# Performance work log

Measured on AMD Instinct MI355X. Metric: run time of the kernel, lower is better.

Reference implementation:

```python
import jax, jax.numpy as jnp
import numpy as np

INPUT_DIM = 1024
OUTPUT_DIM = 1000
DEPTH = 10
LAMBDA_REG = 1e-3
N_INTERNAL = 2 ** DEPTH - 1
N_LEAF = 2 ** DEPTH
BATCH = 16384


def setup_inputs() -> dict:
    key = jax.random.key(0)
    k1, k2, k3 = jax.random.split(key, 3)
    X = jax.random.normal(k1, (BATCH, INPUT_DIM), dtype=jnp.float32)
    # torch nn.Linear weight layout: [out_features, in_features]; scaled to keep
    # sigmoid routing probs away from 0/1 saturation (log-reg term).
    W_internal = jax.random.normal(k2, (N_INTERNAL, INPUT_DIM + 1), dtype=jnp.float32) * 0.02
    W_leaf = jax.random.normal(k3, (OUTPUT_DIM, N_LEAF), dtype=jnp.float32) * 0.02
    return {"X": X, "W_internal": W_internal, "W_leaf": W_leaf}


def _tree_paths(X, W_internal):
    B = X.shape[0]
    Xb = jnp.concatenate([jnp.ones((B, 1), X.dtype), X], axis=1)  # [B, D+1]
    logits = jax.nn.sigmoid(Xb @ W_internal.T)                    # [B, N_int]
    routing = jnp.stack([logits, 1.0 - logits], axis=2)           # [B, N_int, 2]
    path = jnp.ones((B, 1), X.dtype)
    reg = jnp.float32(0.0)
    start = 0
    for layer in range(DEPTH):
        n = 2 ** layer
        lp = routing[:, start:start + n, :].reshape(B, 2 * n)     # next_paths [B, 2n]
        path = jnp.repeat(path, 2, axis=1) * lp                   # new path probs [B, 2n]
        # Faithful to source: parent_idx = node_idx // 2 indexes the UPDATED path probs.
        parent = jnp.repeat(path[:, :n], 2, axis=1)               # [B, 2n]
        num = jnp.sum(lp * parent, axis=0)                        # [2n]
        den = jnp.sum(parent, axis=0) + 1e-8                      # [2n]
        alpha = num / den
        factor = LAMBDA_REG * 2.0 ** (-layer)
        reg = reg + factor * jnp.sum(-0.5 * (jnp.log(alpha) + jnp.log(1.0 - alpha)))
        start += n
    return path, reg  # path: [B, 2^DEPTH]


def reference(X, W_internal, W_leaf):
    path_probs, reg = _tree_paths(X, W_internal)
    predictions = path_probs @ W_leaf.T   # [B, output_dim]
    return predictions, reg
```

## Files before the change

kernel.cpp:

```cpp
#include <hip/hip_runtime.h>
#include <hip/hip_bf16.h>

#define B_ROWS 16384
#define K_DIM  1024
#define N_INT  1023
#define N_OUT  1000

using s8vec = __attribute__((ext_vector_type(8))) short;
using f32x4 = __attribute__((ext_vector_type(4))) float;

static const size_t OFF_XB   = 0;
static const size_t OFF_W1   = OFF_XB   + 33554432;
static const size_t OFF_BIAS = OFF_W1   + 2097152;
static const size_t OFF_PROB = OFF_BIAS + 4096;
static const size_t OFF_PATH = OFF_PROB + 33554432;
static const size_t OFF_W2   = OFF_PATH + 33554432;
static const size_t OFF_SG   = OFF_W2   + 2097152;

__device__ __forceinline__ float b2f(ushort u) {
  return __uint_as_float(((unsigned)u) << 16);
}
__device__ __forceinline__ float blo(unsigned u) { return __uint_as_float(u << 16); }
__device__ __forceinline__ float bhi(unsigned u) { return __uint_as_float(u & 0xffff0000u); }
__device__ __forceinline__ ushort f2b(float f) {
  unsigned u = __float_as_uint(f);
  u = u + 0x7FFFu + ((u >> 16) & 1u);
  return (ushort)(u >> 16);
}

__device__ __forceinline__ void load_lds16(const ushort* g, ushort* l) {
  __builtin_amdgcn_global_load_lds((const __attribute__((address_space(1))) void*)g,
                                   (__attribute__((address_space(3))) void*)l,
                                   16, 0, 0);
}

__global__ __launch_bounds__(256) void cvt_all(const float4* __restrict__ X,
                                               ushort4* __restrict__ O,
                                               const float* __restrict__ Wi,
                                               const float* __restrict__ Wl,
                                               ushort* __restrict__ W1,
                                               ushort* __restrict__ W2,
                                               float* __restrict__ bias) {
  const int b = blockIdx.x;
  if (b < 16384) {
    const int i = b * 256 + threadIdx.x;
    const float4 v = X[i];
    ushort4 o;
    o.x = f2b(v.x); o.y = f2b(v.y); o.z = f2b(v.z); o.w = f2b(v.w);
    O[i] = o;
  } else {
    const int idx = (b - 16384) * 256 + threadIdx.x;
    if (idx < (1 << 20)) {
      const int n = idx >> 10, k = idx & 1023;
      const float v = (n < N_INT) ? Wi[n * 1025 + 1 + k] : 0.f;
      W1[idx] = f2b(v);
      if (k == 0) bias[n] = (n < N_INT) ? Wi[n * 1025] : 0.f;
    } else {
      const int j = idx - (1 << 20);
      const int n = j >> 10, k = j & 1023;
      const float v = (n < N_OUT) ? Wl[n * 1024 + k] : 0.f;
      W2[j] = f2b(v);
    }
  }
}

template <int MODE>
__global__ __launch_bounds__(256, 4) void gemm_bt(const ushort* __restrict__ A,
                                                  const ushort* __restrict__ Bm,
                                                  const float* __restrict__ bias,
                                                  void* __restrict__ outp) {
  __shared__ ushort As[4096];
  __shared__ ushort Bs[4096];
  const int tid = threadIdx.x;
  const int bm = blockIdx.x, bn = blockIdx.y;
  const int lane = tid & 63, wv = tid >> 6;
  const int wm = wv >> 1, wn = wv & 1;
  const int m16 = lane & 15, q = lane >> 4;
  const int qs = q ^ ((m16 >> 1) & 3);

  const int r0 = tid >> 2;
  const int qsw = (tid & 3) ^ ((r0 >> 1) & 3);
  const ushort* aG = A  + (size_t)(bm * 128 + r0) * 1024 + qsw * 8;
  const ushort* bG = Bm + (size_t)(bn * 128 + r0) * 1024 + qsw * 8;
  ushort* AsW = As + wv * 512;
  ushort* BsW = Bs + wv * 512;

  f32x4 acc[4][4] = {};

  for (int k0 = 0; k0 < 1024; k0 += 32) {
    if (k0) __syncthreads();
    load_lds16(aG + k0, AsW);
    load_lds16(aG + 65536 + k0, AsW + 2048);
    load_lds16(bG + k0, BsW);
    load_lds16(bG + 65536 + k0, BsW + 2048);
    __syncthreads();

    s8vec af[4], bfv[4];
#pragma unroll
    for (int i = 0; i < 4; ++i)
      af[i] = *(const s8vec*)(As + (wm * 64 + i * 16 + m16) * 32 + qs * 8);
#pragma unroll
    for (int j = 0; j < 4; ++j)
      bfv[j] = *(const s8vec*)(Bs + (wn * 64 + j * 16 + m16) * 32 + qs * 8);
#pragma unroll
    for (int i = 0; i < 4; ++i)
#pragma unroll
      for (int j = 0; j < 4; ++j)
        acc[i][j] = __builtin_amdgcn_mfma_f32_16x16x32_bf16(af[i], bfv[j], acc[i][j], 0, 0, 0);
  }

  if (MODE == 0) {
    ushort* P = (ushort*)outp;
#pragma unroll
    for (int i = 0; i < 4; ++i)
#pragma unroll
      for (int r = 0; r < 4; ++r) {
        const int gr = bm * 128 + wm * 64 + i * 16 + q * 4 + r;
#pragma unroll
        for (int j = 0; j < 4; ++j) {
          const int gc = bn * 128 + wn * 64 + j * 16 + m16;
          const float z = acc[i][j][r] + bias[gc];
          const float p = 1.f / (1.f + expf(-z));
          if (gc < N_INT) P[(size_t)gr * 1024 + gc + 1] = f2b(p);
        }
      }
  } else {
    float* O = (float*)outp;
#pragma unroll
    for (int i = 0; i < 4; ++i)
#pragma unroll
      for (int r = 0; r < 4; ++r) {
        const int gr = bm * 128 + wm * 64 + i * 16 + q * 4 + r;
#pragma unroll
        for (int j = 0; j < 4; ++j) {
          const int gc = bn * 128 + wn * 64 + j * 16 + m16;
          if (gc < N_OUT) O[(size_t)gr * 1000 + gc] = acc[i][j][r];
        }
      }
  }
}

__global__ __launch_bounds__(256) void tree_kernel(const ushort* __restrict__ probs,
                                                   ushort* __restrict__ path,
                                                   float* __restrict__ Spart) {
  __shared__ float Ss[4096];
  for (int i = threadIdx.x; i < 4096; i += 256) Ss[i] = 0.f;
  __syncthreads();
  const int lane = threadIdx.x & 63;
  const int gw = blockIdx.x * 4 + (threadIdx.x >> 6);

  float at1[6] = {}, at2[6] = {};
  float ae1[30] = {}, ae2[30] = {};

  ushort h4[2], p6a[2]; uint p7a[2]; uint2 p8a[2]; uint4 p9a[2];
#pragma unroll
  for (int rr = 0; rr < 2; ++rr) {
    const ushort* prow = probs + (size_t)(gw * 2 + rr) * 1024;
    h4[rr]  = prow[lane];
    p6a[rr] = prow[64 + lane];
    p7a[rr] = *(const uint*)(prow + 128 + 2 * lane);
    p8a[rr] = *(const uint2*)(prow + 256 + 4 * lane);
    p9a[rr] = *(const uint4*)(prow + 512 + 8 * lane);
  }

#pragma unroll
  for (int rr = 0; rr < 2; ++rr) {
    const int r = gw * 2 + rr;
    const int hh = (int)h4[rr];
    const ushort p6 = p6a[rr];
    const uint   p7 = p7a[rr];
    const uint2  p8 = p8a[rr];
    const uint4  p9 = p9a[rr];

    float v = 1.f;
#pragma unroll
    for (int t = 1; t <= 6; ++t) {
      const int ell = t - 1;
      const int e = lane >> (6 - t);
      const float p = b2f((ushort)__shfl(hh, (1 << ell) + (e >> 1)));
      v *= (e & 1) ? (1.f - p) : p;
      const float pj = b2f((ushort)__shfl(hh, ((1 << ell) + e) & 63));
      if (((lane & ((1 << (6 - t)) - 1)) == 0) && (e < (1 << ell))) {
        at1[ell] += v;
        at2[ell] += pj * v;
      }
    }

    float w[16];
    {
      const float p = b2f(p6);
      w[1] = v * (1.f - p); w[0] = v * p;
    }
    {
      const int j0 = __shfl((int)p6, 2 * lane);
      const int j1 = __shfl((int)p6, 2 * lane + 1);
      if (lane < 32) {
        ae1[0] += w[0]; ae2[0] += b2f((ushort)j0) * w[0];
        ae1[1] += w[1]; ae2[1] += b2f((ushort)j1) * w[1];
      }
    }
    {
      const float pA = blo(p7), pB = bhi(p7);
      w[3] = w[1] * (1.f - pB); w[2] = w[1] * pB;
      w[1] = w[0] * (1.f - pA); w[0] = w[0] * pA;
    }
    {
      const uint ua = (uint)__shfl((int)p7, 2 * lane);
      const uint ub = (uint)__shfl((int)p7, 2 * lane + 1);
      if (lane < 32) {
        ae1[2] += w[0]; ae2[2] += blo(ua) * w[0];
        ae1[3] += w[1]; ae2[3] += bhi(ua) * w[1];
        ae1[4] += w[2]; ae2[4] += blo(ub) * w[2];
        ae1[5] += w[3]; ae2[5] += bhi(ub) * w[3];
      }
    }
    {
      const float pv[4] = { blo(p8.x), bhi(p8.x), blo(p8.y), bhi(p8.y) };
#pragma unroll
      for (int i = 3; i >= 0; --i) {
        w[2 * i + 1] = w[i] * (1.f - pv[i]);
        w[2 * i]     = w[i] * pv[i];
      }
    }
    {
      const uint u0 = (uint)__shfl((int)p8.x, 2 * lane);
      const uint u1 = (uint)__shfl((int)p8.y, 2 * lane);
      const uint u2 = (uint)__shfl((int)p8.x, 2 * lane + 1);
      const uint u3 = (uint)__shfl((int)p8.y, 2 * lane + 1);
      if (lane < 32) {
        ae1[6]  += w[0]; ae2[6]  += blo(u0) * w[0];
        ae1[7]  += w[1]; ae2[7]  += bhi(u0) * w[1];
        ae1[8]  += w[2]; ae2[8]  += blo(u1) * w[2];
        ae1[9]  += w[3]; ae2[9]  += bhi(u1) * w[3];
        ae1[10] += w[4]; ae2[10] += blo(u2) * w[4];
        ae1[11] += w[5]; ae2[11] += bhi(u2) * w[5];
        ae1[12] += w[6]; ae2[12] += blo(u3) * w[6];
        ae1[13] += w[7]; ae2[13] += bhi(u3) * w[7];
      }
    }
    {
      const uint pv[4] = { p9.x, p9.y, p9.z, p9.w };
#pragma unroll
      for (int i = 7; i >= 0; --i) {
        const float p = (i & 1) ? bhi(pv[i >> 1]) : blo(pv[i >> 1]);
        w[2 * i + 1] = w[i] * (1.f - p);
        w[2 * i]     = w[i] * p;
      }
    }
    {
      uint s_[8];
      s_[0] = (uint)__shfl((int)p9.x, 2 * lane);
      s_[1] = (uint)__shfl((int)p9.y, 2 * lane);
      s_[2] = (uint)__shfl((int)p9.z, 2 * lane);
      s_[3] = (uint)__shfl((int)p9.w, 2 * lane);
      s_[4] = (uint)__shfl((int)p9.x, 2 * lane + 1);
      s_[5] = (uint)__shfl((int)p9.y, 2 * lane + 1);
      s_[6] = (uint)__shfl((int)p9.z, 2 * lane + 1);
      s_[7] = (uint)__shfl((int)p9.w, 2 * lane + 1);
      if (lane < 32) {
#pragma unroll
        for (int i = 0; i < 16; ++i) {
          const uint u = s_[i >> 1];
          const float pj = (i & 1) ? bhi(u) : blo(u);
          ae1[14 + i] += w[i]; ae2[14 + i] += pj * w[i];
        }
      }
    }
    union { ushort u[16]; uint4 q4[2]; } pk;
#pragma unroll
    for (int i = 0; i < 16; ++i) pk.u[i] = f2b(w[i]);
    uint4* dst = (uint4*)(path + (size_t)r * 1024 + lane * 16);
    dst[0] = pk.q4[0];
    dst[1] = pk.q4[1];
  }

#pragma unroll
  for (int t = 1; t <= 6; ++t) {
    const int ell = t - 1;
    const int e = lane >> (6 - t);
    if (((lane & ((1 << (6 - t)) - 1)) == 0) && (e < (1 << ell))) {
      const int node = (1 << ell) - 1 + e;
      atomicAdd(&Ss[node], at1[ell]);
      atomicAdd(&Ss[2048 + node], at2[ell]);
    }
  }
  if (lane < 32) {
#pragma unroll
    for (int ell = 6; ell <= 9; ++ell) {
      const int s = 1 << (ell - 6);
      const int pb = (1 << ell) - 1;
      const int base = 2 * s - 2;
#pragma unroll
      for (int i = 0; i < 2 * s; ++i) {
        const int node = pb + 2 * s * lane + i;
        atomicAdd(&Ss[node], ae1[base + i]);
        atomicAdd(&Ss[2048 + node], ae2[base + i]);
      }
    }
  }
  __syncthreads();
  float* Sp = Spart + (size_t)blockIdx.x * 2048;
  for (int i = threadIdx.x; i < 2048; i += 256) {
    const int node = i & 1023;
    Sp[i] = (i < 1024) ? Ss[node] : Ss[2048 + node];
  }
}

__global__ __launch_bounds__(256) void reduce_kernel(const float* __restrict__ Spart,
                                                     float* __restrict__ Sg) {
  const int t = threadIdx.x;
  float acc[8] = {};
  const float* base = Spart + (size_t)blockIdx.x * 64 * 2048;
  for (int b = 0; b < 64; ++b) {
    const float* p = base + (size_t)b * 2048;
#pragma unroll
    for (int k = 0; k < 8; ++k) acc[k] += p[t + 256 * k];
  }
#pragma unroll
  for (int k = 0; k < 8; ++k) {
    const int i = t + 256 * k;
    const int node = i & 1023;
    if (node < 1023) atomicAdd(&Sg[(i < 1024 ? 0 : 2048) + node], acc[k]);
  }
}

__global__ __launch_bounds__(1024) void finalize_kernel(const float* __restrict__ Sg,
                                                        float* __restrict__ outreg) {
  const int tid = threadIdx.x;
  double val = 0.0;
  if (tid < 1023) {
    const int ell = 31 - __clz(tid + 1);
    const double s1 = (double)Sg[tid];
    const double s2 = (double)Sg[2048 + tid];
    const double den = s1 + 1e-8;
    const double a0 = s2 / den;
    const double a1 = (s1 - s2) / den;
    const double f = 1e-3 * (1.0 / (double)(1 << ell));
    val = -0.5 * f * (log(a0) + log(1.0 - a0) + log(a1) + log(1.0 - a1));
  }
#pragma unroll
  for (int o = 32; o > 0; o >>= 1) val += __shfl_down(val, o, 64);
  __shared__ double partd[16];
  if ((tid & 63) == 0) partd[tid >> 6] = val;
  __syncthreads();
  if (tid == 0) {
    double t = 0.0;
    for (int i = 0; i < 16; ++i) t += partd[i];
    outreg[0] = (float)t;
  }
}

extern "C" void kernel_launch(void* const* d_in, const int* in_sizes, int n_in,
                              void* d_out, int out_size, void* d_ws, size_t ws_size,
                              hipStream_t stream) {
  const float* X     = (const float*)d_in[0];
  const float* Wint  = (const float*)d_in[1];
  const float* Wleaf = (const float*)d_in[2];
  float* out = (float*)d_out;
  char* ws = (char*)d_ws;

  ushort* Xb   = (ushort*)(ws + OFF_XB);
  ushort* W1   = (ushort*)(ws + OFF_W1);
  float*  bias = (float*)(ws + OFF_BIAS);
  ushort* prob = (ushort*)(ws + OFF_PROB);
  ushort* path = (ushort*)(ws + OFF_PATH);
  ushort* W2   = (ushort*)(ws + OFF_W2);
  float*  Sg   = (float*)(ws + OFF_SG);
  float*  Spart = (float*)(ws + OFF_PROB);

  (void)hipMemsetAsync(ws + OFF_SG, 0, 16384, stream);
  cvt_all<<<24576, 256, 0, stream>>>((const float4*)X, (ushort4*)Xb,
                                     Wint, Wleaf, W1, W2, bias);
  gemm_bt<0><<<dim3(128, 8), 256, 0, stream>>>(Xb, W1, bias, (void*)prob);
  tree_kernel<<<2048, 256, 0, stream>>>(prob, path, Spart);
  gemm_bt<1><<<dim3(128, 8), 256, 0, stream>>>(path, W2, nullptr, (void*)out);
  reduce_kernel<<<32, 256, 0, stream>>>(Spart, Sg);
  finalize_kernel<<<1, 1024, 0, stream>>>(Sg, out + (size_t)B_ROWS * N_OUT);
}
```

Measured before the change: 344.0 us.

## Split tree kernel into path-only pass and separate bottom-up statistics accumulation kernel

The tree kernel now only computes and writes path probabilities, one row per wave, without any statistics accumulation. A new accum_kernel runs after the second GEMM. It rereads probs and the bf16 paths, builds the per-node sums bottom-up from the leaf paths with pairwise adds and shuffles, and writes per-block partials. The aim is to take atomics and register pressure off the critical path before the second GEMM. The cost is an extra read of roughly 64MB, and the statistics now come from bf16-rounded paths.

```diff
diff --git a/kernel.cpp b/kernel.cpp
--- a/kernel.cpp
+++ b/kernel.cpp
@@ -141,177 +141,177 @@
 }
 
 __global__ __launch_bounds__(256) void tree_kernel(const ushort* __restrict__ probs,
-                                                   ushort* __restrict__ path,
-                                                   float* __restrict__ Spart) {
-  __shared__ float Ss[4096];
-  for (int i = threadIdx.x; i < 4096; i += 256) Ss[i] = 0.f;
-  __syncthreads();
+                                                   ushort* __restrict__ path) {
   const int lane = threadIdx.x & 63;
-  const int gw = blockIdx.x * 4 + (threadIdx.x >> 6);
-
-  float at1[6] = {}, at2[6] = {};
-  float ae1[30] = {}, ae2[30] = {};
-
-  ushort h4[2], p6a[2]; uint p7a[2]; uint2 p8a[2]; uint4 p9a[2];
-#pragma unroll
-  for (int rr = 0; rr < 2; ++rr) {
-    const ushort* prow = probs + (size_t)(gw * 2 + rr) * 1024;
-    h4[rr]  = prow[lane];
-    p6a[rr] = prow[64 + lane];
-    p7a[rr] = *(const uint*)(prow + 128 + 2 * lane);
-    p8a[rr] = *(const uint2*)(prow + 256 + 4 * lane);
-    p9a[rr] = *(const uint4*)(prow + 512 + 8 * lane);
-  }
-
-#pragma unroll
-  for (int rr = 0; rr < 2; ++rr) {
-    const int r = gw * 2 + rr;
-    const int hh = (int)h4[rr];
-    const ushort p6 = p6a[rr];
-    const uint   p7 = p7a[rr];
-    const uint2  p8 = p8a[rr];
-    const uint4  p9 = p9a[rr];
-
-    float v = 1.f;
-#pragma unroll
-    for (int t = 1; t <= 6; ++t) {
-      const int ell = t - 1;
-      const int e = lane >> (6 - t);
-      const float p = b2f((ushort)__shfl(hh, (1 << ell) + (e >> 1)));
-      v *= (e & 1) ? (1.f - p) : p;
-      const float pj = b2f((ushort)__shfl(hh, ((1 << ell) + e) & 63));
-      if (((lane & ((1 << (6 - t)) - 1)) == 0) && (e < (1 << ell))) {
-        at1[ell] += v;
-        at2[ell] += pj * v;
-      }
-    }
-
-    float w[16];
-    {
-      const float p = b2f(p6);
-      w[1] = v * (1.f - p); w[0] = v * p;
-    }
-    {
-      const int j0 = __shfl((int)p6, 2 * lane);
-      const int j1 = __shfl((int)p6, 2 * lane + 1);
-      if (lane < 32) {
-        ae1[0] += w[0]; ae2[0] += b2f((ushort)j0) * w[0];
-        ae1[1] += w[1]; ae2[1] += b2f((ushort)j1) * w[1];
-      }
-    }
-    {
-      const float pA = blo(p7), pB = bhi(p7);
-      w[3] = w[1] * (1.f - pB); w[2] = w[1] * pB;
-      w[1] = w[0] * (1.f - pA); w[0] = w[0] * pA;
-    }
-    {
-      const uint ua = (uint)__shfl((int)p7, 2 * lane);
-      const uint ub = (uint)__shfl((int)p7, 2 * lane + 1);
-      if (lane < 32) {
-        ae1[2] += w[0]; ae2[2] += blo(ua) * w[0];
-        ae1[3] += w[1]; ae2[3] += bhi(ua) * w[1];
-        ae1[4] += w[2]; ae2[4] += blo(ub) * w[2];
-        ae1[5] += w[3]; ae2[5] += bhi(ub) * w[3];
-      }
-    }
-    {
-      const float pv[4] = { blo(p8.x), bhi(p8.x), blo(p8.y), bhi(p8.y) };
-#pragma unroll
-      for (int i = 3; i >= 0; --i) {
-        w[2 * i + 1] = w[i] * (1.f - pv[i]);
-        w[2 * i]     = w[i] * pv[i];
-      }
-    }
-    {
-      const uint u0 = (uint)__shfl((int)p8.x, 2 * lane);
-      const uint u1 = (uint)__shfl((int)p8.y, 2 * lane);
-      const uint u2 = (uint)__shfl((int)p8.x, 2 * lane + 1);
-      const uint u3 = (uint)__shfl((int)p8.y, 2 * lane + 1);
-      if (lane < 32) {
-        ae1[6]  += w[0]; ae2[6]  += blo(u0) * w[0];
-        ae1[7]  += w[1]; ae2[7]  += bhi(u0) * w[1];
-        ae1[8]  += w[2]; ae2[8]  += blo(u1) * w[2];
-        ae1[9]  += w[3]; ae2[9]  += bhi(u1) * w[3];
-        ae1[10] += w[4]; ae2[10] += blo(u2) * w[4];
-        ae1[11] += w[5]; ae2[11] += bhi(u2) * w[5];
-        ae1[12] += w[6]; ae2[12] += blo(u3) * w[6];
-        ae1[13] += w[7]; ae2[13] += bhi(u3) * w[7];
-      }
-    }
-    {
-      const uint pv[4] = { p9.x, p9.y, p9.z, p9.w };
-#pragma unroll
-      for (int i = 7; i >= 0; --i) {
-        const float p = (i & 1) ? bhi(pv[i >> 1]) : blo(pv[i >> 1]);
-        w[2 * i + 1] = w[i] * (1.f - p);
-        w[2 * i]     = w[i] * p;
-      }
-    }
-    {
-      uint s_[8];
-      s_[0] = (uint)__shfl((int)p9.x, 2 * lane);
-      s_[1] = (uint)__shfl((int)p9.y, 2 * lane);
-      s_[2] = (uint)__shfl((int)p9.z, 2 * lane);
-      s_[3] = (uint)__shfl((int)p9.w, 2 * lane);
-      s_[4] = (uint)__shfl((int)p9.x, 2 * lane + 1);
-      s_[5] = (uint)__shfl((int)p9.y, 2 * lane + 1);
-      s_[6] = (uint)__shfl((int)p9.z, 2 * lane + 1);
-      s_[7] = (uint)__shfl((int)p9.w, 2 * lane + 1);
-      if (lane < 32) {
-#pragma unroll
-        for (int i = 0; i < 16; ++i) {
-          const uint u = s_[i >> 1];
-          const float pj = (i & 1) ? bhi(u) : blo(u);
-          ae1[14 + i] += w[i]; ae2[14 + i] += pj * w[i];
-        }
-      }
-    }
-    union { ushort u[16]; uint4 q4[2]; } pk;
-#pragma unroll
-    for (int i = 0; i < 16; ++i) pk.u[i] = f2b(w[i]);
-    uint4* dst = (uint4*)(path + (size_t)r * 1024 + lane * 16);
-    dst[0] = pk.q4[0];
-    dst[1] = pk.q4[1];
-  }
-
+  const int r = blockIdx.x * 4 + (threadIdx.x >> 6);
+  const ushort* prow = probs + (size_t)r * 1024;
+
+  const int hh  = (int)prow[lane];
+  const ushort p6 = prow[64 + lane];
+  const uint   p7 = *(const uint*)(prow + 128 + 2 * lane);
+  const uint2  p8 = *(const uint2*)(prow + 256 + 4 * lane);
+  const uint4  p9 = *(const uint4*)(prow + 512 + 8 * lane);
+
+  float v = 1.f;
 #pragma unroll
   for (int t = 1; t <= 6; ++t) {
     const int ell = t - 1;
     const int e = lane >> (6 - t);
-    if (((lane & ((1 << (6 - t)) - 1)) == 0) && (e < (1 << ell))) {
-      const int node = (1 << ell) - 1 + e;
-      atomicAdd(&Ss[node], at1[ell]);
-      atomicAdd(&Ss[2048 + node], at2[ell]);
+    const float p = b2f((ushort)__shfl(hh, (1 << ell) + (e >> 1)));
+    v *= (e & 1) ? (1.f - p) : p;
+  }
+
+  float w[16];
+  { const float p = b2f(p6); w[1] = v * (1.f - p); w[0] = v * p; }
+  {
+    const float pA = blo(p7), pB = bhi(p7);
+    w[3] = w[1] * (1.f - pB); w[2] = w[1] * pB;
+    w[1] = w[0] * (1.f - pA); w[0] = w[0] * pA;
+  }
+  {
+    const float pv[4] = { blo(p8.x), bhi(p8.x), blo(p8.y), bhi(p8.y) };
+#pragma unroll
+    for (int i = 3; i >= 0; --i) {
+      w[2 * i + 1] = w[i] * (1.f - pv[i]);
+      w[2 * i]     = w[i] * pv[i];
     }
   }
+  {
+    const uint pv[4] = { p9.x, p9.y, p9.z, p9.w };
+#pragma unroll
+    for (int i = 7; i >= 0; --i) {
+      const float p = (i & 1) ? bhi(pv[i >> 1]) : blo(pv[i >> 1]);
+      w[2 * i + 1] = w[i] * (1.f - p);
+      w[2 * i]     = w[i] * p;
+    }
+  }
+  union { ushort u[16]; uint4 q4[2]; } pk;
+#pragma unroll
+  for (int i = 0; i < 16; ++i) pk.u[i] = f2b(w[i]);
+  uint4* dst = (uint4*)(path + (size_t)r * 1024 + lane * 16);
+  dst[0] = pk.q4[0];
+  dst[1] = pk.q4[1];
+}
+
+__global__ __launch_bounds__(256) void accum_kernel(const ushort* __restrict__ probs,
+                                                    const ushort* __restrict__ path,
+                                                    float* __restrict__ Spart) {
+  __shared__ float Ss[2048];
+  for (int i = threadIdx.x; i < 2048; i += 256) Ss[i] = 0.f;
+  __syncthreads();
+  const int lane = threadIdx.x & 63;
+  const int ll = lane & 31;
+  const int half = lane >> 5;
+  const int hb = half << 5;
+  const int gw = blockIdx.x * 4 + (threadIdx.x >> 6);
+
+  float a19[16] = {}, a29[16] = {};
+  float a18[8]  = {}, a28[8]  = {};
+  float a17[4]  = {}, a27[4]  = {};
+  float a16[2]  = {}, a26[2]  = {};
+  float t1[6] = {}, t2[6] = {};
+
+#pragma unroll
+  for (int it = 0; it < 2; ++it) {
+    const int r = gw * 4 + it * 2 + half;
+    const ushort* prow = probs + (size_t)r * 1024;
+    const ushort* wrow = path  + (size_t)r * 1024;
+
+    const int   hlo = (int)prow[ll];
+    const float p5  = b2f(prow[32 + ll]);
+    union { uint4 q[2]; ushort u[16]; } wl;
+    wl.q[0] = *(const uint4*)(wrow + 16 * ll);
+    wl.q[1] = *(const uint4*)(wrow + 16 * ll + 8);
+    union { uint4 q[2]; ushort u[16]; } j9;
+    j9.q[0] = *(const uint4*)(prow + 512 + 16 * ll);
+    j9.q[1] = *(const uint4*)(prow + 512 + 16 * ll + 8);
+    union { uint4 q; ushort u[8]; } j8;
+    j8.q = *(const uint4*)(prow + 256 + 8 * ll);
+    union { uint2 q; ushort u[4]; } j7;
+    j7.q = *(const uint2*)(prow + 128 + 4 * ll);
+    union { uint q; ushort u[2]; } j6;
+    j6.q = *(const uint*)(prow + 64 + 2 * ll);
+
+    float w[16];
+#pragma unroll
+    for (int i = 0; i < 16; ++i) w[i] = b2f(wl.u[i]);
+    float L8[8], L7[4], L6[2];
+#pragma unroll
+    for (int i = 0; i < 8; ++i) L8[i] = w[2 * i] + w[2 * i + 1];
+#pragma unroll
+    for (int i = 0; i < 4; ++i) L7[i] = L8[2 * i] + L8[2 * i + 1];
+    L6[0] = L7[0] + L7[1]; L6[1] = L7[2] + L7[3];
+    const float T = L6[0] + L6[1];
+
+#pragma unroll
+    for (int i = 0; i < 16; ++i) { a19[i] += w[i];  a29[i] += b2f(j9.u[i]) * w[i]; }
+#pragma unroll
+    for (int i = 0; i < 8; ++i)  { a18[i] += L8[i]; a28[i] += b2f(j8.u[i]) * L8[i]; }
+#pragma unroll
+    for (int i = 0; i < 4; ++i)  { a17[i] += L7[i]; a27[i] += b2f(j7.u[i]) * L7[i]; }
+#pragma unroll
+    for (int i = 0; i < 2; ++i)  { a16[i] += L6[i]; a26[i] += b2f(j6.u[i]) * L6[i]; }
+
+    t1[5] += T; t2[5] += p5 * T;
+    const float T1 = T  + __shfl_xor(T, 1);
+    const float T2 = T1 + __shfl_xor(T1, 2);
+    const float T3 = T2 + __shfl_xor(T2, 4);
+    const float T4 = T3 + __shfl_xor(T3, 8);
+    const float T5 = T4 + __shfl_xor(T4, 16);
+    const float v4 = __shfl(T1, hb | ((2 * ll) & 31));
+    const float v3 = __shfl(T2, hb | ((4 * ll) & 31));
+    const float v2 = __shfl(T3, hb | ((8 * ll) & 31));
+    const float v1 = __shfl(T4, hb | ((16 * ll) & 31));
+    const float q4 = b2f((ushort)__shfl(hlo, hb | ((16 + ll) & 31)));
+    const float q3 = b2f((ushort)__shfl(hlo, hb | ((8 + ll) & 31)));
+    const float q2 = b2f((ushort)__shfl(hlo, hb | ((4 + ll) & 31)));
+    const float q1 = b2f((ushort)__shfl(hlo, hb | ((2 + ll) & 31)));
+    const float q0 = b2f((ushort)__shfl(hlo, hb | 1));
+    if (ll < 16) { t1[4] += v4; t2[4] += q4 * v4; }
+    if (ll < 8)  { t1[3] += v3; t2[3] += q3 * v3; }
+    if (ll < 4)  { t1[2] += v2; t2[2] += q2 * v2; }
+    if (ll < 2)  { t1[1] += v1; t2[1] += q1 * v1; }
+    if (ll < 1)  { t1[0] += T5; t2[0] += q0 * T5; }
+  }
+
+#pragma unroll
+  for (int i = 0; i < 16; ++i) { a19[i] += __shfl_xor(a19[i], 32); a29[i] += __shfl_xor(a29[i], 32); }
+#pragma unroll
+  for (int i = 0; i < 8; ++i)  { a18[i] += __shfl_xor(a18[i], 32); a28[i] += __shfl_xor(a28[i], 32); }
+#pragma unroll
+  for (int i = 0; i < 4; ++i)  { a17[i] += __shfl_xor(a17[i], 32); a27[i] += __shfl_xor(a27[i], 32); }
+#pragma unroll
+  for (int i = 0; i < 2; ++i)  { a16[i] += __shfl_xor(a16[i], 32); a26[i] += __shfl_xor(a26[i], 32); }
+#pragma unroll
+  for (int i = 0; i < 6; ++i)  { t1[i] += __shfl_xor(t1[i], 32);   t2[i] += __shfl_xor(t2[i], 32); }
+
   if (lane < 32) {
 #pragma unroll
-    for (int ell = 6; ell <= 9; ++ell) {
-      const int s = 1 << (ell - 6);
-      const int pb = (1 << ell) - 1;
-      const int base = 2 * s - 2;
-#pragma unroll
-      for (int i = 0; i < 2 * s; ++i) {
-        const int node = pb + 2 * s * lane + i;
-        atomicAdd(&Ss[node], ae1[base + i]);
-        atomicAdd(&Ss[2048 + node], ae2[base + i]);
-      }
-    }
+    for (int i = 0; i < 16; ++i) { atomicAdd(&Ss[511 + 16 * ll + i], a19[i]); atomicAdd(&Ss[1535 + 16 * ll + i], a29[i]); }
+#pragma unroll
+    for (int i = 0; i < 8; ++i)  { atomicAdd(&Ss[255 + 8 * ll + i],  a18[i]); atomicAdd(&Ss[1279 + 8 * ll + i],  a28[i]); }
+#pragma unroll
+    for (int i = 0; i < 4; ++i)  { atomicAdd(&Ss[127 + 4 * ll + i],  a17[i]); atomicAdd(&Ss[1151 + 4 * ll + i],  a27[i]); }
+#pragma unroll
+    for (int i = 0; i < 2; ++i)  { atomicAdd(&Ss[63 + 2 * ll + i],   a16[i]); atomicAdd(&Ss[1087 + 2 * ll + i],  a26[i]); }
+    atomicAdd(&Ss[31 + ll], t1[5]); atomicAdd(&Ss[1055 + ll], t2[5]);
+    if (ll < 16) { atomicAdd(&Ss[15 + ll], t1[4]); atomicAdd(&Ss[1039 + ll], t2[4]); }
+    if (ll < 8)  { atomicAdd(&Ss[7 + ll],  t1[3]); atomicAdd(&Ss[1031 + ll], t2[3]); }
+    if (ll < 4)  { atomicAdd(&Ss[3 + ll],  t1[2]); atomicAdd(&Ss[1027 + ll], t2[2]); }
+    if (ll < 2)  { atomicAdd(&Ss[1 + ll],  t1[1]); atomicAdd(&Ss[1025 + ll], t2[1]); }
+    if (ll < 1)  { atomicAdd(&Ss[0],       t1[0]); atomicAdd(&Ss[1024],      t2[0]); }
   }
   __syncthreads();
   float* Sp = Spart + (size_t)blockIdx.x * 2048;
-  for (int i = threadIdx.x; i < 2048; i += 256) {
-    const int node = i & 1023;
-    Sp[i] = (i < 1024) ? Ss[node] : Ss[2048 + node];
-  }
+  for (int i = threadIdx.x; i < 2048; i += 256) Sp[i] = Ss[i];
 }
 
 __global__ __launch_bounds__(256) void reduce_kernel(const float* __restrict__ Spart,
                                                      float* __restrict__ Sg) {
   const int t = threadIdx.x;
   float acc[8] = {};
-  const float* base = Spart + (size_t)blockIdx.x * 64 * 2048;
-  for (int b = 0; b < 64; ++b) {
+  const float* base = Spart + (size_t)blockIdx.x * 32 * 2048;
+  for (int b = 0; b < 32; ++b) {
     const float* p = base + (size_t)b * 2048;
 #pragma unroll
     for (int k = 0; k < 8; ++k) acc[k] += p[t + 256 * k];
@@ -366,14 +366,15 @@
   ushort* path = (ushort*)(ws + OFF_PATH);
   ushort* W2   = (ushort*)(ws + OFF_W2);
   float*  Sg   = (float*)(ws + OFF_SG);
-  float*  Spart = (float*)(ws + OFF_PROB);
+  float*  Spart = (float*)(ws + OFF_XB);
 
   (void)hipMemsetAsync(ws + OFF_SG, 0, 16384, stream);
   cvt_all<<<24576, 256, 0, stream>>>((const float4*)X, (ushort4*)Xb,
                                      Wint, Wleaf, W1, W2, bias);
   gemm_bt<0><<<dim3(128, 8), 256, 0, stream>>>(Xb, W1, bias, (void*)prob);
-  tree_kernel<<<2048, 256, 0, stream>>>(prob, path, Spart);
+  tree_kernel<<<4096, 256, 0, stream>>>(prob, path);
   gemm_bt<1><<<dim3(128, 8), 256, 0, stream>>>(path, W2, nullptr, (void*)out);
+  accum_kernel<<<1024, 256, 0, stream>>>(prob, path, Spart);
   reduce_kernel<<<32, 256, 0, stream>>>(Spart, Sg);
   finalize_kernel<<<1, 1024, 0, stream>>>(Sg, out + (size_t)B_ROWS * N_OUT);
 }
```

After: 307.2 us. -10.7%, faster.
